# Performance work log

Measured on AMD Instinct MI355X. Metric: run time of the kernel, lower is better.

The kernel has to match this reference:

```python
import jax, jax.numpy as jnp
import numpy as np

DECAY = 0.99
EPSILON = 1e-05
N_TOKENS = 32768
EMBED_DIM = 256
NUM_EMB = 4096


def setup_inputs() -> dict:
    key = jax.random.key(0)
    k1, k2, k3 = jax.random.split(key, 3)
    return {
        "inputs": jax.random.normal(k1, (N_TOKENS, EMBED_DIM), dtype=jnp.float32),
        "codebook": jax.random.normal(k2, (NUM_EMB, EMBED_DIM), dtype=jnp.float32),
        "ema_w": jax.random.normal(k3, (NUM_EMB, EMBED_DIM), dtype=jnp.float32),
        "ema_cluster_size": jnp.zeros((NUM_EMB,), dtype=jnp.float32),
    }


def reference(inputs, codebook, ema_w, ema_cluster_size):
    K, D = codebook.shape
    flat = inputs.reshape(-1, D)  # [N, D]
    distances = (
        jnp.sum(flat * flat, axis=1, keepdims=True)
        + jnp.sum(codebook * codebook, axis=1)
        - 2.0 * flat @ codebook.T
    )
    encoding_indices = jnp.argmin(distances, axis=1)  # [N]
    encodings = jax.nn.one_hot(encoding_indices, K, dtype=flat.dtype)  # [N, K]
    quantized = codebook[encoding_indices].reshape(inputs.shape)  # [N, D]

    # EMA update (training branch). dw = encodings.T @ flat expressed as a
    # segment sum to avoid a second [N,K]-sized contraction pass.
    dw = jax.ops.segment_sum(flat, encoding_indices, num_segments=K)  # [K, D]
    counts = jax.ops.segment_sum(
        jnp.ones((flat.shape[0],), dtype=flat.dtype), encoding_indices, num_segments=K
    )  # [K]
    new_ema_w = ema_w * DECAY + (1.0 - DECAY) * dw
    cs = ema_cluster_size * DECAY + (1.0 - DECAY) * counts
    n = jnp.sum(cs)
    cs = (cs + EPSILON) / (n + K * EPSILON) * n  # laplace smoothing
    new_codebook = new_ema_w / cs[:, None]
    return quantized, encodings, new_codebook, new_ema_w, cs
```

## Files before the change

kernel.cpp:

```cpp
#include <hip/hip_runtime.h>
#include <hip/hip_bf16.h>

#define NTOK 32768
#define KEMB 4096
#define DDIM 256
#define DECAYF 0.99f
#define EPSF 1e-5f
#define KSPLIT 256
#define FLAG_THETA 0.09f
#define PRUNE_MARGIN 0.25f

#define B_AHAT  0ull
#define B_BHAT  16777216ull
#define B_PART  18874368ull
#define B_CE    52428800ull
#define B_CNTI  52445184ull
#define B_CSP   52461568ull
#define B_OFFS  52477952ull
#define B_NPTR  52494336ull
#define B_TIDX  52494400ull
#define B_FLIST 52625472ull
#define B_SLOT  52756544ull
#define B_TLIST 52887616ull
#define B_DW    53018688ull

#define OFF_Q  0ull
#define OFF_E  8388608ull
#define OFF_CB 142606336ull
#define OFF_W  143654912ull
#define OFF_CS 144703488ull

typedef __attribute__((ext_vector_type(8))) _Float16 f16x8;
typedef __attribute__((ext_vector_type(4))) _Float16 f16x4;
typedef __attribute__((ext_vector_type(4))) float f32x4;

__global__ __launch_bounds__(256) void cast16_kernel(const float* __restrict__ src,
                                                     _Float16* __restrict__ dst) {
    size_t gid = (size_t)blockIdx.x * 256 + threadIdx.x;
    const float* sp = src + gid * 8;
    f16x8 v;
    #pragma unroll
    for (int t = 0; t < 8; ++t) v[t] = (_Float16)sp[t];
    *(f16x8*)(dst + gid * 8) = v;
}

__global__ __launch_bounds__(256) void castcb_ce_kernel(const float* __restrict__ cb,
                                                        _Float16* __restrict__ Bhat,
                                                        float* __restrict__ ce) {
    int k = blockIdx.x * 4 + (threadIdx.x >> 6);
    int lane = threadIdx.x & 63;
    float4 v = *(const float4*)(cb + (size_t)k * DDIM + lane * 4);
    f16x4 h;
    h[0] = (_Float16)v.x; h[1] = (_Float16)v.y;
    h[2] = (_Float16)v.z; h[3] = (_Float16)v.w;
    *(f16x4*)(Bhat + (size_t)k * DDIM + lane * 4) = h;
    float s = v.x * v.x + v.y * v.y + v.z * v.z + v.w * v.w;
    #pragma unroll
    for (int o = 32; o > 0; o >>= 1) s += __shfl_down(s, o);
    if (lane == 0) ce[k] = s;
}

__global__ __launch_bounds__(256) void gemm_argmin_kernel(
        const _Float16* __restrict__ Ahat,
        const _Float16* __restrict__ Bhat,
        const float* __restrict__ ceg,
        float4* __restrict__ part) {
    __shared__ _Float16 As[128 * 64];
    __shared__ _Float16 Bs[128 * 64];
    const int tid  = threadIdx.x;
    const int lane = tid & 63;
    const int wave = tid >> 6;
    const int wm = wave >> 1, wn = wave & 1;

    int lin = blockIdx.y * 32 + blockIdx.x;
    lin = (lin & 7) * 1024 + (lin >> 3);
    const int nb = lin & 31, mb = lin >> 5;

    const int col = lane & 15, q = lane >> 4;
    const int cswz = q ^ (col & 7);

    const int srow = tid >> 3;
    const int sswz = (tid & 7) ^ (srow & 7);
    const _Float16* ag = Ahat + (size_t)(mb * 128 + srow) * KSPLIT + sswz * 8;
    const _Float16* bg = Bhat + (size_t)(nb * 128 + srow) * KSPLIT + sswz * 8;

    f32x4 zero = {0.f, 0.f, 0.f, 0.f};
    f32x4 acc[4][4];
    #pragma unroll
    for (int i = 0; i < 4; ++i)
        #pragma unroll
        for (int j = 0; j < 4; ++j) acc[i][j] = zero;

    for (int kt = 0; kt < KSPLIT / 64; ++kt) {
        __syncthreads();
        #pragma unroll
        for (int n = 0; n < 4; ++n) {
            __builtin_amdgcn_global_load_lds(
                (const __attribute__((address_space(1))) void*)(ag + (size_t)n * 32 * KSPLIT + kt * 64),
                (__attribute__((address_space(3))) void*)(As + n * 2048 + tid * 8), 16, 0, 0);
            __builtin_amdgcn_global_load_lds(
                (const __attribute__((address_space(1))) void*)(bg + (size_t)n * 32 * KSPLIT + kt * 64),
                (__attribute__((address_space(3))) void*)(Bs + n * 2048 + tid * 8), 16, 0, 0);
        }
        __syncthreads();

        const f16x8* Av = (const f16x8*)As;
        const f16x8* Bv = (const f16x8*)Bs;
        #pragma unroll
        for (int ks = 0; ks < 2; ++ks) {
            f16x8 a[4], b[4];
            #pragma unroll
            for (int i = 0; i < 4; ++i)
                a[i] = Av[(wm * 64 + i * 16 + col) * 8 + (cswz ^ (ks * 4))];
            #pragma unroll
            for (int j = 0; j < 4; ++j)
                b[j] = Bv[(wn * 64 + j * 16 + col) * 8 + (cswz ^ (ks * 4))];
            #pragma unroll
            for (int i = 0; i < 4; ++i)
                #pragma unroll
                for (int j = 0; j < 4; ++j)
                    acc[i][j] = __builtin_amdgcn_mfma_f32_16x16x32_f16(a[i], b[j], acc[i][j], 0, 0, 0);
        }
    }

    float ce_j[4];
    #pragma unroll
    for (int j = 0; j < 4; ++j) ce_j[j] = ceg[nb * 128 + wn * 64 + j * 16 + col];

    #pragma unroll
    for (int i = 0; i < 4; ++i) {
        #pragma unroll
        for (int r = 0; r < 4; ++r) {
            float b1 = 3.4e38f, b2 = 3.4e38f;
            int i1 = 0x7fffffff;
            #pragma unroll
            for (int j = 0; j < 4; ++j) {
                float s = ce_j[j] - 2.0f * acc[i][j][r];
                int n = nb * 128 + wn * 64 + j * 16 + col;
                if (s < b1) { b2 = b1; b1 = s; i1 = n; }
                else if (s < b2) { b2 = s; }
            }
            #pragma unroll
            for (int m = 1; m < 16; m <<= 1) {
                float ob1 = __shfl_xor(b1, m, 16);
                float ob2 = __shfl_xor(b2, m, 16);
                int   oi  = __shfl_xor(i1, m, 16);
                bool take = (ob1 < b1) || (ob1 == b1 && oi < i1);
                float nb2 = take ? fminf(b1, ob2) : fminf(b2, ob1);
                if (take) { b1 = ob1; i1 = oi; }
                b2 = nb2;
            }
            if (col == i * 4 + r) {
                int mrow = mb * 128 + wm * 64 + i * 16 + q * 4 + r;
                float4 p;
                p.x = b1; p.y = b2; p.z = __int_as_float(i1); p.w = 0.0f;
                part[(size_t)mrow * 64 + nb * 2 + wn] = p;
            }
        }
    }
}

__global__ __launch_bounds__(256) void argmin_reduce_kernel(
        const float4* __restrict__ part,
        int* __restrict__ tokIdx,
        int* __restrict__ flist,
        int* __restrict__ flagCount) {
    int row = blockIdx.x * 4 + (threadIdx.x >> 6);
    int lane = threadIdx.x & 63;
    float4 p = part[(size_t)row * 64 + lane];
    float b1 = p.x, b2 = p.y;
    int i1 = __float_as_int(p.z);
    #pragma unroll
    for (int m = 1; m < 64; m <<= 1) {
        float ob1 = __shfl_xor(b1, m);
        float ob2 = __shfl_xor(b2, m);
        int   oi  = __shfl_xor(i1, m);
        bool take = (ob1 < b1) || (ob1 == b1 && oi < i1);
        float nb2 = take ? fminf(b1, ob2) : fminf(b2, ob1);
        if (take) { b1 = ob1; i1 = oi; }
        b2 = nb2;
    }
    if (lane == 0) {
        tokIdx[row] = i1;
        if (b2 - b1 < FLAG_THETA) {
            int slot = atomicAdd(flagCount, 1);
            flist[slot] = row;
        }
    }
}

__global__ __launch_bounds__(256) void refine_kernel(const float* __restrict__ xg,
                                                     const float* __restrict__ cb,
                                                     const float4* __restrict__ part,
                                                     int* __restrict__ tokIdx,
                                                     const int* __restrict__ flagList,
                                                     const int* __restrict__ flagCount) {
    int nf = *flagCount;
    int lane = threadIdx.x & 63;
    int wid = (blockIdx.x * 256 + threadIdx.x) >> 6;
    int nw = (gridDim.x * 256) >> 6;
    for (int f = wid; f < nf; f += nw) {
        int tok = flagList[f];
        float cb1 = part[(size_t)tok * 64 + lane].x;
        float b1 = cb1;
        #pragma unroll
        for (int m = 1; m < 64; m <<= 1) b1 = fminf(b1, __shfl_xor(b1, m));
        unsigned long long mask = __ballot(cb1 <= b1 + PRUNE_MARGIN);
        double best = 1e300;
        int bi = 0x7fffffff;
        const float* xr = xg + (size_t)tok * DDIM;
        while (mask) {
            int c = __ffsll(mask) - 1;
            mask &= mask - 1;
            int k = c * 64 + lane;
            const float* e = cb + (size_t)k * DDIM;
            double s = 0.0;
            for (int d4 = 0; d4 < DDIM / 4; ++d4) {
                float4 e4 = *(const float4*)(e + d4 * 4);
                float4 x4 = *(const float4*)(xr + d4 * 4);
                double e0 = (double)e4.x, e1 = (double)e4.y;
                double e2 = (double)e4.z, e3 = (double)e4.w;
                s += e0 * (e0 - 2.0 * (double)x4.x) + e1 * (e1 - 2.0 * (double)x4.y)
                   + e2 * (e2 - 2.0 * (double)x4.z) + e3 * (e3 - 2.0 * (double)x4.w);
            }
            if (s < best || (s == best && k < bi)) { best = s; bi = k; }
        }
        #pragma unroll
        for (int m = 1; m < 64; m <<= 1) {
            double ob = __shfl_xor(best, m);
            int   oi  = __shfl_xor(bi, m);
            if (ob < best || (ob == best && oi < bi)) { best = ob; bi = oi; }
        }
        if (lane == 0) tokIdx[tok] = bi;
    }
}

__global__ __launch_bounds__(256) void finalize_kernel(const float* __restrict__ cb,
                                                       const int* __restrict__ tokIdx,
                                                       int* __restrict__ countsI,
                                                       int* __restrict__ slotOf,
                                                       float* __restrict__ quant,
                                                       float* __restrict__ enc) {
    int t = blockIdx.x * 4 + (threadIdx.x >> 6);
    int lane = threadIdx.x & 63;
    int k = tokIdx[t];
    if (lane == 0) {
        slotOf[t] = atomicAdd(countsI + k, 1);
        enc[(size_t)t * KEMB + k] = 1.0f;
    }
    float4 e = *(const float4*)(cb + (size_t)k * DDIM + lane * 4);
    *(float4*)(quant + (size_t)t * DDIM + lane * 4) = e;
}

__global__ __launch_bounds__(256) void scan_cs_kernel(const int* __restrict__ countsI,
                                                      const float* __restrict__ ema_cs,
                                                      int* __restrict__ offs,
                                                      float* __restrict__ cs_pre,
                                                      float* __restrict__ nptr) {
    __shared__ int part[256];
    __shared__ float npart[256];
    __shared__ int pref[257];
    int tid = threadIdx.x;
    int local[16];
    int s = 0;
    float ns = 0.0f;
    #pragma unroll
    for (int i = 0; i < 16; ++i) {
        int c = countsI[tid * 16 + i];
        local[i] = c;
        s += c;
        float csp = ema_cs[tid * 16 + i] * DECAYF + (1.0f - DECAYF) * (float)c;
        cs_pre[tid * 16 + i] = csp;
        ns += csp;
    }
    part[tid] = s;
    npart[tid] = ns;
    __syncthreads();
    if (tid == 0) {
        pref[0] = 0;
        float nn = 0.0f;
        for (int i = 0; i < 256; ++i) {
            pref[i + 1] = pref[i] + part[i];
            nn += npart[i];
        }
        nptr[0] = nn;
    }
    __syncthreads();
    int run = pref[tid];
    #pragma unroll
    for (int i = 0; i < 16; ++i) { offs[tid * 16 + i] = run; run += local[i]; }
}

__global__ __launch_bounds__(256) void filllist_kernel(const int* __restrict__ tokIdx,
                                                       const int* __restrict__ offs,
                                                       const int* __restrict__ slotOf,
                                                       int* __restrict__ tlist) {
    int t = blockIdx.x * 256 + threadIdx.x;
    int k = tokIdx[t];
    tlist[offs[k] + slotOf[t]] = t;
}

#define SEG_CHUNK 32
__global__ __launch_bounds__(256) void segdw_kernel(const float* __restrict__ xg,
                                                    const int* __restrict__ tlist,
                                                    const int* __restrict__ tokIdx,
                                                    float* __restrict__ dw) {
    int tid = threadIdx.x;
    int s0 = blockIdx.x * SEG_CHUNK;
    float acc = 0.0f;
    int curk = -1;
    for (int s = s0; s < s0 + SEG_CHUNK; ++s) {
        int t = tlist[s];
        int k = tokIdx[t];
        if (k != curk) {
            if (curk >= 0) atomicAdd(dw + (size_t)curk * DDIM + tid, acc);
            acc = 0.0f;
            curk = k;
        }
        acc += xg[(size_t)t * DDIM + tid];
    }
    if (curk >= 0) atomicAdd(dw + (size_t)curk * DDIM + tid, acc);
}

__global__ __launch_bounds__(256) void epi_kernel(const float* __restrict__ ema_w,
                                                  const float* __restrict__ dw,
                                                  const float* __restrict__ cs_pre,
                                                  const float* __restrict__ nptr,
                                                  float* __restrict__ new_cb,
                                                  float* __restrict__ new_w,
                                                  float* __restrict__ cs_out) {
    int gid = blockIdx.x * 256 + threadIdx.x;
    int k = gid >> 8, d = gid & 255;
    float n = *nptr;
    float csp = cs_pre[k];
    float cs = (csp + EPSF) / (n + (float)KEMB * EPSF) * n;
    float w = ema_w[gid] * DECAYF + (1.0f - DECAYF) * dw[gid];
    new_w[gid] = w;
    new_cb[gid] = w / cs;
    if (d == 0) cs_out[k] = cs;
}

extern "C" void kernel_launch(void* const* d_in, const int* in_sizes, int n_in,
                              void* d_out, int out_size, void* d_ws, size_t ws_size,
                              hipStream_t stream) {
    const float* xg     = (const float*)d_in[0];
    const float* cbg    = (const float*)d_in[1];
    const float* ema_w  = (const float*)d_in[2];
    const float* ema_cs = (const float*)d_in[3];

    float* out = (float*)d_out;
    unsigned char* wsb = (unsigned char*)d_ws;

    float* quant  = out + OFF_Q;
    float* enc    = out + OFF_E;
    float* new_cb = out + OFF_CB;
    float* new_w  = out + OFF_W;
    float* cs_out = out + OFF_CS;

    _Float16* Ahat = (_Float16*)(wsb + B_AHAT);
    _Float16* Bhat = (_Float16*)(wsb + B_BHAT);
    float4* part   = (float4*)(wsb + B_PART);
    float* ce      = (float*)(wsb + B_CE);
    int*   countsI = (int*)(wsb + B_CNTI);
    float* cs_pre  = (float*)(wsb + B_CSP);
    int*   offs    = (int*)(wsb + B_OFFS);
    float* nptr    = (float*)(wsb + B_NPTR);
    int*   flagCnt = (int*)(wsb + B_NPTR + 4);
    int*   tokIdx  = (int*)(wsb + B_TIDX);
    int*   flist   = (int*)(wsb + B_FLIST);
    int*   slotOf  = (int*)(wsb + B_SLOT);
    int*   tlist   = (int*)(wsb + B_TLIST);
    float* dw      = (float*)(wsb + B_DW);

    hipMemsetAsync(enc, 0, (size_t)NTOK * KEMB * sizeof(float), stream);
    hipMemsetAsync(countsI, 0, KEMB * sizeof(int), stream);
    hipMemsetAsync(nptr, 0, 8, stream);
    hipMemsetAsync(dw, 0, (size_t)KEMB * DDIM * sizeof(float), stream);

    cast16_kernel<<<(NTOK * DDIM / 8) / 256, 256, 0, stream>>>(xg, Ahat);
    castcb_ce_kernel<<<KEMB / 4, 256, 0, stream>>>(cbg, Bhat, ce);
    gemm_argmin_kernel<<<dim3(KEMB / 128, NTOK / 128), 256, 0, stream>>>(Ahat, Bhat, ce, part);
    argmin_reduce_kernel<<<NTOK / 4, 256, 0, stream>>>(part, tokIdx, flist, flagCnt);
    refine_kernel<<<256, 256, 0, stream>>>(xg, cbg, part, tokIdx, flist, flagCnt);
    finalize_kernel<<<NTOK / 4, 256, 0, stream>>>(cbg, tokIdx, countsI, slotOf, quant, enc);
    scan_cs_kernel<<<1, 256, 0, stream>>>(countsI, ema_cs, offs, cs_pre, nptr);
    filllist_kernel<<<NTOK / 256, 256, 0, stream>>>(tokIdx, offs, slotOf, tlist);
    segdw_kernel<<<NTOK / SEG_CHUNK, 256, 0, stream>>>(xg, tlist, tokIdx, dw);
    epi_kernel<<<(KEMB * DDIM) / 256, 256, 0, stream>>>(ema_w, dw, cs_pre, nptr,
                                                        new_cb, new_w, cs_out);
}
```

Baseline: 835.0 us.

## Fuse prep casts with zeroing, and merge argmin reduce, refine and finalize

The two fp16 cast kernels and the memsets of the counts and dw buffers become one prep kernel that picks its role by block index. The argmin reduction, the fp64 refinement of near-tie tokens and the finalize step (quantized gather, one-hot write, count atomics) become one per-token post kernel. This removes several launches, the global flag list and its atomic counter. Flagged tokens are now refined inside the wave that reduced them, which trades the old compact work list for divergence spread across waves. The memset of nptr is dropped, so the code relies on scan_cs writing that value directly.

```diff
diff --git a/kernel.cpp b/kernel.cpp
--- a/kernel.cpp
+++ b/kernel.cpp
@@ -19,7 +19,6 @@
 #define B_OFFS  52477952ull
 #define B_NPTR  52494336ull
 #define B_TIDX  52494400ull
-#define B_FLIST 52625472ull
 #define B_SLOT  52756544ull
 #define B_TLIST 52887616ull
 #define B_DW    53018688ull
@@ -34,30 +33,40 @@
 typedef __attribute__((ext_vector_type(4))) _Float16 f16x4;
 typedef __attribute__((ext_vector_type(4))) float f32x4;
 
-__global__ __launch_bounds__(256) void cast16_kernel(const float* __restrict__ src,
-                                                     _Float16* __restrict__ dst) {
-    size_t gid = (size_t)blockIdx.x * 256 + threadIdx.x;
-    const float* sp = src + gid * 8;
-    f16x8 v;
-    #pragma unroll
-    for (int t = 0; t < 8; ++t) v[t] = (_Float16)sp[t];
-    *(f16x8*)(dst + gid * 8) = v;
-}
-
-__global__ __launch_bounds__(256) void castcb_ce_kernel(const float* __restrict__ cb,
-                                                        _Float16* __restrict__ Bhat,
-                                                        float* __restrict__ ce) {
-    int k = blockIdx.x * 4 + (threadIdx.x >> 6);
-    int lane = threadIdx.x & 63;
-    float4 v = *(const float4*)(cb + (size_t)k * DDIM + lane * 4);
-    f16x4 h;
-    h[0] = (_Float16)v.x; h[1] = (_Float16)v.y;
-    h[2] = (_Float16)v.z; h[3] = (_Float16)v.w;
-    *(f16x4*)(Bhat + (size_t)k * DDIM + lane * 4) = h;
-    float s = v.x * v.x + v.y * v.y + v.z * v.z + v.w * v.w;
-    #pragma unroll
-    for (int o = 32; o > 0; o >>= 1) s += __shfl_down(s, o);
-    if (lane == 0) ce[k] = s;
+__global__ __launch_bounds__(256) void prep_kernel(const float* __restrict__ xg,
+                                                   const float* __restrict__ cbg,
+                                                   _Float16* __restrict__ Ahat,
+                                                   _Float16* __restrict__ Bhat,
+                                                   float* __restrict__ ce,
+                                                   int* __restrict__ countsI,
+                                                   float4* __restrict__ dwv) {
+    int b = blockIdx.x;
+    int tid = threadIdx.x;
+    if (b < 4096) {
+        size_t gid = (size_t)b * 256 + tid;
+        const float* sp = xg + gid * 8;
+        f16x8 v;
+        #pragma unroll
+        for (int t = 0; t < 8; ++t) v[t] = (_Float16)sp[t];
+        *(f16x8*)(Ahat + gid * 8) = v;
+    } else if (b < 5120) {
+        int k = (b - 4096) * 4 + (tid >> 6);
+        int lane = tid & 63;
+        float4 v = *(const float4*)(cbg + (size_t)k * DDIM + lane * 4);
+        f16x4 h;
+        h[0] = (_Float16)v.x; h[1] = (_Float16)v.y;
+        h[2] = (_Float16)v.z; h[3] = (_Float16)v.w;
+        *(f16x4*)(Bhat + (size_t)k * DDIM + lane * 4) = h;
+        float s = v.x * v.x + v.y * v.y + v.z * v.z + v.w * v.w;
+        #pragma unroll
+        for (int o = 32; o > 0; o >>= 1) s += __shfl_down(s, o);
+        if (lane == 0) ce[k] = s;
+    } else if (b < 5136) {
+        countsI[(b - 5120) * 256 + tid] = 0;
+    } else {
+        float4 z = {0.f, 0.f, 0.f, 0.f};
+        dwv[(size_t)(b - 5136) * 256 + tid] = z;
+    }
 }
 
 __global__ __launch_bounds__(256) void gemm_argmin_kernel(
@@ -160,16 +169,20 @@
     }
 }
 
-__global__ __launch_bounds__(256) void argmin_reduce_kernel(
-        const float4* __restrict__ part,
-        int* __restrict__ tokIdx,
-        int* __restrict__ flist,
-        int* __restrict__ flagCount) {
+__global__ __launch_bounds__(256) void post_kernel(const float* __restrict__ xg,
+                                                   const float* __restrict__ cb,
+                                                   const float4* __restrict__ part,
+                                                   int* __restrict__ tokIdx,
+                                                   int* __restrict__ countsI,
+                                                   int* __restrict__ slotOf,
+                                                   float* __restrict__ quant,
+                                                   float* __restrict__ enc) {
     int row = blockIdx.x * 4 + (threadIdx.x >> 6);
     int lane = threadIdx.x & 63;
     float4 p = part[(size_t)row * 64 + lane];
     float b1 = p.x, b2 = p.y;
     int i1 = __float_as_int(p.z);
+    float cb1 = p.x;
     #pragma unroll
     for (int m = 1; m < 64; m <<= 1) {
         float ob1 = __shfl_xor(b1, m);
@@ -180,35 +193,12 @@
         if (take) { b1 = ob1; i1 = oi; }
         b2 = nb2;
     }
-    if (lane == 0) {
-        tokIdx[row] = i1;
-        if (b2 - b1 < FLAG_THETA) {
-            int slot = atomicAdd(flagCount, 1);
-            flist[slot] = row;
-        }
-    }
-}
-
-__global__ __launch_bounds__(256) void refine_kernel(const float* __restrict__ xg,
-                                                     const float* __restrict__ cb,
-                                                     const float4* __restrict__ part,
-                                                     int* __restrict__ tokIdx,
-                                                     const int* __restrict__ flagList,
-                                                     const int* __restrict__ flagCount) {
-    int nf = *flagCount;
-    int lane = threadIdx.x & 63;
-    int wid = (blockIdx.x * 256 + threadIdx.x) >> 6;
-    int nw = (gridDim.x * 256) >> 6;
-    for (int f = wid; f < nf; f += nw) {
-        int tok = flagList[f];
-        float cb1 = part[(size_t)tok * 64 + lane].x;
-        float b1 = cb1;
-        #pragma unroll
-        for (int m = 1; m < 64; m <<= 1) b1 = fminf(b1, __shfl_xor(b1, m));
+    int kfin = i1;
+    if (b2 - b1 < FLAG_THETA) {
         unsigned long long mask = __ballot(cb1 <= b1 + PRUNE_MARGIN);
         double best = 1e300;
         int bi = 0x7fffffff;
-        const float* xr = xg + (size_t)tok * DDIM;
+        const float* xr = xg + (size_t)row * DDIM;
         while (mask) {
             int c = __ffsll(mask) - 1;
             mask &= mask - 1;
@@ -231,25 +221,15 @@
             int   oi  = __shfl_xor(bi, m);
             if (ob < best || (ob == best && oi < bi)) { best = ob; bi = oi; }
         }
-        if (lane == 0) tokIdx[tok] = bi;
-    }
-}
-
-__global__ __launch_bounds__(256) void finalize_kernel(const float* __restrict__ cb,
-                                                       const int* __restrict__ tokIdx,
-                                                       int* __restrict__ countsI,
-                                                       int* __restrict__ slotOf,
-                                                       float* __restrict__ quant,
-                                                       float* __restrict__ enc) {
-    int t = blockIdx.x * 4 + (threadIdx.x >> 6);
-    int lane = threadIdx.x & 63;
-    int k = tokIdx[t];
+        kfin = bi;
+    }
     if (lane == 0) {
-        slotOf[t] = atomicAdd(countsI + k, 1);
-        enc[(size_t)t * KEMB + k] = 1.0f;
-    }
-    float4 e = *(const float4*)(cb + (size_t)k * DDIM + lane * 4);
-    *(float4*)(quant + (size_t)t * DDIM + lane * 4) = e;
+        tokIdx[row] = kfin;
+        slotOf[row] = atomicAdd(countsI + kfin, 1);
+        enc[(size_t)row * KEMB + kfin] = 1.0f;
+    }
+    float4 e = *(const float4*)(cb + (size_t)kfin * DDIM + lane * 4);
+    *(float4*)(quant + (size_t)row * DDIM + lane * 4) = e;
 }
 
 __global__ __launch_bounds__(256) void scan_cs_kernel(const int* __restrict__ countsI,
@@ -365,24 +345,16 @@
     float* cs_pre  = (float*)(wsb + B_CSP);
     int*   offs    = (int*)(wsb + B_OFFS);
     float* nptr    = (float*)(wsb + B_NPTR);
-    int*   flagCnt = (int*)(wsb + B_NPTR + 4);
     int*   tokIdx  = (int*)(wsb + B_TIDX);
-    int*   flist   = (int*)(wsb + B_FLIST);
     int*   slotOf  = (int*)(wsb + B_SLOT);
     int*   tlist   = (int*)(wsb + B_TLIST);
     float* dw      = (float*)(wsb + B_DW);
 
     hipMemsetAsync(enc, 0, (size_t)NTOK * KEMB * sizeof(float), stream);
-    hipMemsetAsync(countsI, 0, KEMB * sizeof(int), stream);
-    hipMemsetAsync(nptr, 0, 8, stream);
-    hipMemsetAsync(dw, 0, (size_t)KEMB * DDIM * sizeof(float), stream);
-
-    cast16_kernel<<<(NTOK * DDIM / 8) / 256, 256, 0, stream>>>(xg, Ahat);
-    castcb_ce_kernel<<<KEMB / 4, 256, 0, stream>>>(cbg, Bhat, ce);
+
+    prep_kernel<<<6160, 256, 0, stream>>>(xg, cbg, Ahat, Bhat, ce, countsI, (float4*)dw);
     gemm_argmin_kernel<<<dim3(KEMB / 128, NTOK / 128), 256, 0, stream>>>(Ahat, Bhat, ce, part);
-    argmin_reduce_kernel<<<NTOK / 4, 256, 0, stream>>>(part, tokIdx, flist, flagCnt);
-    refine_kernel<<<256, 256, 0, stream>>>(xg, cbg, part, tokIdx, flist, flagCnt);
-    finalize_kernel<<<NTOK / 4, 256, 0, stream>>>(cbg, tokIdx, countsI, slotOf, quant, enc);
+    post_kernel<<<NTOK / 4, 256, 0, stream>>>(xg, cbg, part, tokIdx, countsI, slotOf, quant, enc);
     scan_cs_kernel<<<1, 256, 0, stream>>>(countsI, ema_cs, offs, cs_pre, nptr);
     filllist_kernel<<<NTOK / 256, 256, 0, stream>>>(tokIdx, offs, slotOf, tlist);
     segdw_kernel<<<NTOK / SEG_CHUNK, 256, 0, stream>>>(xg, tlist, tokIdx, dw);
```

Result: faster. 804.3 us (-3.7%).
